# Optimization experiments

Measured on AMD Instinct MI355X. Metric: run time of the kernel, lower is better.

## Reference

```python
import jax, jax.numpy as jnp
import numpy as np
import math

D_MODEL = 2048
N_HEADS = 16
HEAD_DIM = D_MODEL // N_HEADS
ROPE_THETA = 10000.0
EPS = 1e-5


def _rope_cos_sin(seq_len, dim, theta):
    inv_freq = 1.0 / theta ** (jnp.arange(0, dim, 2, dtype=jnp.float32) / dim)  # [dim/2]
    t = jnp.arange(seq_len, dtype=jnp.float32)
    freqs = jnp.outer(t, inv_freq)  # [S, dim/2]
    return jnp.cos(freqs), jnp.sin(freqs)


def _apply_rope(x, cos, sin):
    # x: [B, S, H, D]; pairs (even, odd) rotated by angle freqs[s, d/2]
    xs = x.reshape(x.shape[:-1] + (x.shape[-1] // 2, 2))
    x0, x1 = xs[..., 0], xs[..., 1]
    c = cos[None, :, None, :]
    s = sin[None, :, None, :]
    out = jnp.stack([x0 * c - x1 * s, x0 * s + x1 * c], axis=-1)
    return out.reshape(x.shape)


def _layernorm(x, w, eps):
    # LayerNorm over last dim, no bias
    mu = jnp.mean(x, axis=-1, keepdims=True)
    var = jnp.mean(jnp.square(x - mu), axis=-1, keepdims=True)
    return (x - mu) * jax.lax.rsqrt(var + eps) * w


def setup_inputs() -> dict:
    key = jax.random.key(0)
    ks = jax.random.split(key, 5)
    B, S = 2, 2048
    w_std = math.sqrt(1.0 / D_MODEL)  # ~xavier for square matrices
    return {
        "x": jax.random.normal(ks[0], (B, S, D_MODEL), dtype=jnp.float32),
        "wq": jax.random.normal(ks[1], (D_MODEL, D_MODEL), dtype=jnp.float32) * w_std,
        "wk": jax.random.normal(ks[2], (D_MODEL, D_MODEL), dtype=jnp.float32) * w_std,
        "wv": jax.random.normal(ks[3], (D_MODEL, D_MODEL), dtype=jnp.float32) * w_std,
        "wo": jax.random.normal(ks[4], (D_MODEL, D_MODEL), dtype=jnp.float32) * w_std,
        "q_norm_w": jnp.ones((HEAD_DIM,), dtype=jnp.float32),
        "k_norm_w": jnp.ones((HEAD_DIM,), dtype=jnp.float32),
        "window_size": 1024,
    }


def reference(x, wq, wk, wv, wo, q_norm_w, k_norm_w, window_size):
    B, S, _ = x.shape
    # bias-free projections (torch Linear: x @ W.T)
    q = (x @ wq.T).reshape(B, S, N_HEADS, HEAD_DIM)
    k = (x @ wk.T).reshape(B, S, N_HEADS, HEAD_DIM)
    v = (x @ wv.T).reshape(B, S, N_HEADS, HEAD_DIM)

    cos, sin = _rope_cos_sin(S, HEAD_DIM, ROPE_THETA)
    q = _apply_rope(q, cos, sin)
    k = _apply_rope(k, cos, sin)

    # per-head QK LayerNorm (no bias)
    q = _layernorm(q, q_norm_w, EPS)
    k = _layernorm(k, k_norm_w, EPS)

    scale = 1.0 / math.sqrt(HEAD_DIM)
    scores = jnp.einsum("bqhd,bkhd->bhqk", q, k) * scale  # [B,H,S,S]

    # sliding-window causal mask: attend to j in [i - window, i]
    i = jnp.arange(S)[:, None]
    j = jnp.arange(S)[None, :]
    allowed = (j <= i) & (j >= i - window_size)
    scores = jnp.where(allowed, scores, -jnp.inf)

    attn = jax.nn.softmax(scores, axis=-1)
    out = jnp.einsum("bhqk,bkhd->bqhd", attn, v).reshape(B, S, D_MODEL)
    return out @ wo.T
```

## Files before the change

### kernel.cpp

```cpp
#include <hip/hip_runtime.h>

typedef __bf16 bfv8 __attribute__((ext_vector_type(8)));
typedef float f32x4 __attribute__((ext_vector_type(4)));

#define DMODEL 2048
#define NHEADS 16
#define HEADD 128
#define SEQ 2048
#define BATCH 2
#define MROWS (BATCH * SEQ)

__device__ __forceinline__ unsigned short f2bf(float f) {
    unsigned int x = __float_as_uint(f);
    x += 0x7fffu + ((x >> 16) & 1u);
    return (unsigned short)(x >> 16);
}
__device__ __forceinline__ float bf2f(unsigned short u) {
    return __uint_as_float((unsigned int)u << 16);
}
__device__ __forceinline__ unsigned int pk2(float a, float b) {
    return (unsigned int)f2bf(a) | ((unsigned int)f2bf(b) << 16);
}

__global__ __launch_bounds__(256) void cvt_f2b(const float* __restrict__ s,
                                               unsigned short* __restrict__ d, int n) {
    int i = (blockIdx.x * 256 + threadIdx.x) * 4;
    if (i >= n) return;
    float4 v = *(const float4*)(s + i);
    ushort4 o;
    o.x = f2bf(v.x); o.y = f2bf(v.y); o.z = f2bf(v.z); o.w = f2bf(v.w);
    *(ushort4*)(d + i) = o;
}

template <int CPRL>
__device__ __forceinline__ void stage_t(const unsigned short* __restrict__ gbase,
                                        unsigned short* lds, size_t strideShorts,
                                        int wave, int lane) {
#pragma unroll
    for (int i = 0; i < 4; ++i) {
        int L = wave * 256 + i * 64 + lane;
        int m = L >> CPRL, c = L & ((1 << CPRL) - 1);
        int g = c ^ (m & 7);
        const unsigned short* gp = gbase + (size_t)m * strideShorts + g * 8;
        __builtin_amdgcn_global_load_lds(
            (const __attribute__((address_space(1))) unsigned int*)gp,
            (__attribute__((address_space(3))) unsigned int*)(lds + (size_t)(wave * 256 + i * 64) * 8),
            16, 0, 0);
    }
}

#define GBK 64

__global__ __launch_bounds__(256) void gemm_qkv(const unsigned short* __restrict__ A,
                                                const unsigned short* __restrict__ Bw,
                                                unsigned short* __restrict__ Qb,
                                                unsigned short* __restrict__ Kb,
                                                unsigned short* __restrict__ VT) {
    __shared__ __align__(16) unsigned short As[128 * 64];
    __shared__ __align__(16) unsigned short Bs[128 * 64];
    const int K = DMODEL;
    int tid  = threadIdx.x;
    int bm   = blockIdx.y * 128, bn = blockIdx.x * 128;
    int wave = tid >> 6, lane = tid & 63;
    int wm   = (wave >> 1) * 64, wn = (wave & 1) * 64;
    int lr   = lane & 15, lg = lane >> 4;

    f32x4 acc[4][4];
    f32x4 z = {0.f, 0.f, 0.f, 0.f};
#pragma unroll
    for (int i = 0; i < 4; ++i)
#pragma unroll
        for (int j = 0; j < 4; ++j) acc[i][j] = z;

    const unsigned short* Ab = A  + (size_t)bm * K;
    const unsigned short* Bb = Bw + (size_t)bn * K;

    for (int k0 = 0; k0 < K; k0 += GBK) {
        __syncthreads();
        stage_t<3>(Ab + k0, As, K, wave, lane);
        stage_t<3>(Bb + k0, Bs, K, wave, lane);
        __syncthreads();
#pragma unroll
        for (int kk = 0; kk < GBK; kk += 32) {
            int ck = (kk >> 3) + lg;
            bfv8 af[4], bf[4];
#pragma unroll
            for (int i = 0; i < 4; ++i)
                af[i] = *(const bfv8*)&As[(wm + i * 16 + lr) * 64 + ((ck ^ (lr & 7))) * 8];
#pragma unroll
            for (int j = 0; j < 4; ++j)
                bf[j] = *(const bfv8*)&Bs[(wn + j * 16 + lr) * 64 + ((ck ^ (lr & 7))) * 8];
#pragma unroll
            for (int i = 0; i < 4; ++i)
#pragma unroll
                for (int j = 0; j < 4; ++j)
                    acc[i][j] = __builtin_amdgcn_mfma_f32_16x16x32_bf16(af[i], bf[j], acc[i][j], 0, 0, 0);
        }
    }
    int orow0 = bm + wm + lg * 4;
    int region = bn >> 11;
    int nloc   = bn & 2047;
    if (region < 2) {
        unsigned short* C = region ? Kb : Qb;
#pragma unroll
        for (int i = 0; i < 4; ++i)
#pragma unroll
            for (int j = 0; j < 4; ++j)
#pragma unroll
                for (int r = 0; r < 4; ++r)
                    C[(size_t)(orow0 + i * 16 + r) * DMODEL + nloc + wn + j * 16 + lr] = f2bf(acc[i][j][r]);
    } else {
#pragma unroll
        for (int i = 0; i < 4; ++i) {
            int row = orow0 + i * 16;
            int bb = row >> 11, ss = row & (SEQ - 1);
#pragma unroll
            for (int j = 0; j < 4; ++j) {
                int col = nloc + wn + j * 16 + lr;
                int hh = col >> 7, dd = col & (HEADD - 1);
                ushort4 o4;
                o4.x = f2bf(acc[i][j][0]);
                o4.y = f2bf(acc[i][j][1]);
                o4.z = f2bf(acc[i][j][2]);
                o4.w = f2bf(acc[i][j][3]);
                *(ushort4*)(VT + ((size_t)((bb * NHEADS + hh) * HEADD + dd)) * SEQ + ss) = o4;
            }
        }
    }
}

__global__ __launch_bounds__(256) void gemm_bt(const unsigned short* __restrict__ A,
                                               const unsigned short* __restrict__ Bw,
                                               float* __restrict__ C,
                                               int M, int N, int K) {
    __shared__ __align__(16) unsigned short As[128 * 64];
    __shared__ __align__(16) unsigned short Bs[128 * 64];
    int tid  = threadIdx.x;
    int bm   = blockIdx.y * 128, bn = blockIdx.x * 128;
    int wave = tid >> 6, lane = tid & 63;
    int wm   = (wave >> 1) * 64, wn = (wave & 1) * 64;
    int lr   = lane & 15, lg = lane >> 4;

    f32x4 acc[4][4];
    f32x4 z = {0.f, 0.f, 0.f, 0.f};
#pragma unroll
    for (int i = 0; i < 4; ++i)
#pragma unroll
        for (int j = 0; j < 4; ++j) acc[i][j] = z;

    const unsigned short* Ab = A  + (size_t)bm * K;
    const unsigned short* Bb = Bw + (size_t)bn * K;

    for (int k0 = 0; k0 < K; k0 += GBK) {
        __syncthreads();
        stage_t<3>(Ab + k0, As, K, wave, lane);
        stage_t<3>(Bb + k0, Bs, K, wave, lane);
        __syncthreads();
#pragma unroll
        for (int kk = 0; kk < GBK; kk += 32) {
            int ck = (kk >> 3) + lg;
            bfv8 af[4], bf[4];
#pragma unroll
            for (int i = 0; i < 4; ++i)
                af[i] = *(const bfv8*)&As[(wm + i * 16 + lr) * 64 + ((ck ^ (lr & 7))) * 8];
#pragma unroll
            for (int j = 0; j < 4; ++j)
                bf[j] = *(const bfv8*)&Bs[(wn + j * 16 + lr) * 64 + ((ck ^ (lr & 7))) * 8];
#pragma unroll
            for (int i = 0; i < 4; ++i)
#pragma unroll
                for (int j = 0; j < 4; ++j)
                    acc[i][j] = __builtin_amdgcn_mfma_f32_16x16x32_bf16(af[i], bf[j], acc[i][j], 0, 0, 0);
        }
    }
    int orow0 = bm + wm + lg * 4;
    int ocol0 = bn + wn + lr;
#pragma unroll
    for (int i = 0; i < 4; ++i)
#pragma unroll
        for (int j = 0; j < 4; ++j)
#pragma unroll
            for (int r = 0; r < 4; ++r)
                C[(size_t)(orow0 + i * 16 + r) * N + ocol0 + j * 16] = acc[i][j][r];
}

__global__ __launch_bounds__(256) void rope_ln_ip(unsigned short* __restrict__ qt,
                                                  unsigned short* __restrict__ kt,
                                                  const float* __restrict__ qw,
                                                  const float* __restrict__ kw) {
    int which = blockIdx.y;
    unsigned short* t = which ? kt : qt;
    const float* w = which ? kw : qw;
    float scale = which ? 1.0f : 0.08838834764831845f;
    int gr   = blockIdx.x * 4 + (threadIdx.x >> 6);
    int lane = threadIdx.x & 63;
    int m = gr >> 4;
    int h = gr & 15;
    int s = m & (SEQ - 1);
    unsigned short* p = t + (size_t)m * DMODEL + h * HEADD + lane * 2;
    ushort2 xv = *(const ushort2*)p;
    float x0 = bf2f(xv.x), x1 = bf2f(xv.y);
    float inv = powf(10000.0f, -(float)lane * (1.0f / 64.0f));
    float ang = (float)s * inv;
    float sn, c;
    sincosf(ang, &sn, &c);
    float y0 = x0 * c - x1 * sn;
    float y1 = x0 * sn + x1 * c;
    float sum = y0 + y1;
    float sq  = y0 * y0 + y1 * y1;
#pragma unroll
    for (int o = 32; o >= 1; o >>= 1) {
        sum += __shfl_xor(sum, o);
        sq  += __shfl_xor(sq, o);
    }
    float mu  = sum * (1.0f / 128.0f);
    float var = sq * (1.0f / 128.0f) - mu * mu;
    float rs  = rsqrtf(var + 1e-5f) * scale;
    float2 wv = *(const float2*)(w + lane * 2);
    ushort2 ov;
    ov.x = f2bf((y0 - mu) * rs * wv.x);
    ov.y = f2bf((y1 - mu) * rs * wv.y);
    *(ushort2*)p = ov;
}

#define AQT 64
#define AKT 64

__global__ __launch_bounds__(256) void attn_mfma(const unsigned short* __restrict__ qb,
                                                 const unsigned short* __restrict__ kb,
                                                 const unsigned short* __restrict__ vt,
                                                 unsigned short* __restrict__ ob,
                                                 const int* __restrict__ wptr) {
    __shared__ __align__(16) unsigned short Ks[64 * 128];
    __shared__ __align__(16) unsigned short Vs[128 * 64];
    __shared__ __align__(16) unsigned short Ps[4 * 16 * 64];
    int tid  = threadIdx.x;
    int wq   = tid >> 6, lane = tid & 63;
    int lm   = lane & 15, lg = lane >> 4;
    int lm7  = lm & 7;
    int gid  = blockIdx.x;
    int xcd  = gid & 7, slot = gid >> 3;
    int bh   = xcd * 4 + (slot >> 5);
    int b    = bh >> 4, h = bh & 15;
    int q0   = (31 - (slot & 31)) * AQT;
    int W    = *wptr;
    unsigned short* PsW = &Ps[wq * 1024];

    bfv8 qa[4];
    {
        const unsigned short* qp = qb + (size_t)(b * SEQ + q0 + wq * 16 + lm) * DMODEL + h * HEADD + lg * 8;
#pragma unroll
        for (int kk = 0; kk < 4; ++kk) qa[kk] = *(const bfv8*)(qp + kk * 32);
    }

    f32x4 o[8];
    f32x4 z = {0.f, 0.f, 0.f, 0.f};
#pragma unroll
    for (int n = 0; n < 8; ++n) o[n] = z;
    float mrow = -1e30f, lrow = 0.f;

    const unsigned short* kbase = kb + (size_t)(b * SEQ) * DMODEL + h * HEADD;
    const unsigned short* vbase = vt + (size_t)((b * NHEADS + h) * HEADD) * SEQ;

    int kt_lo = max(0, q0 - W) & ~(AKT - 1);
    int qi = q0 + wq * 16 + lm;

    for (int kt = kt_lo; kt < q0 + AQT; kt += AKT) {
        __syncthreads();
        stage_t<4>(kbase + (size_t)kt * DMODEL, Ks, DMODEL, wq, lane);
        stage_t<3>(vbase + kt, Vs, SEQ, wq, lane);
        __syncthreads();

        f32x4 s[4];
#pragma unroll
        for (int j = 0; j < 4; ++j) s[j] = z;
#pragma unroll
        for (int kk = 0; kk < 4; ++kk) {
#pragma unroll
            for (int j = 0; j < 4; ++j) {
                int ck = (kk * 4 + lg) ^ lm7;
                bfv8 af = *(const bfv8*)&Ks[(j * 16 + lm) * 128 + ck * 8];
                s[j] = __builtin_amdgcn_mfma_f32_16x16x32_bf16(af, qa[kk], s[j], 0, 0, 0);
            }
        }
        if ((kt + 63 >= q0) || (kt < q0 + 63 - W)) {
#pragma unroll
            for (int j = 0; j < 4; ++j) {
                int kj0 = kt + j * 16 + lg * 4;
#pragma unroll
                for (int r = 0; r < 4; ++r) {
                    bool ok = (kj0 + r <= qi) && (kj0 + r >= qi - W);
                    s[j][r] = ok ? s[j][r] : -1e30f;
                }
            }
        }
        float mx = -1e30f;
#pragma unroll
        for (int j = 0; j < 4; ++j)
#pragma unroll
            for (int r = 0; r < 4; ++r) mx = fmaxf(mx, s[j][r]);
        mx = fmaxf(mx, __shfl_xor(mx, 16));
        mx = fmaxf(mx, __shfl_xor(mx, 32));
        float mnew  = fmaxf(mrow, mx);
        float alpha = __expf(mrow - mnew);
        mrow = mnew;
        float ls = 0.f;
#pragma unroll
        for (int j = 0; j < 4; ++j) {
            float p0 = __expf(s[j][0] - mnew);
            float p1 = __expf(s[j][1] - mnew);
            float p2 = __expf(s[j][2] - mnew);
            float p3 = __expf(s[j][3] - mnew);
            ls += (p0 + p1) + (p2 + p3);
            int c0 = (j * 2 + (lg >> 1)) ^ lm7;
            uint2 wv;
            wv.x = pk2(p0, p1);
            wv.y = pk2(p2, p3);
            *(uint2*)&PsW[lm * 64 + c0 * 8 + (lg & 1) * 4] = wv;
        }
        ls += __shfl_xor(ls, 16);
        ls += __shfl_xor(ls, 32);
        lrow = lrow * alpha + ls;
        float al[4];
#pragma unroll
        for (int r = 0; r < 4; ++r) al[r] = __shfl(alpha, lg * 4 + r);
#pragma unroll
        for (int n = 0; n < 8; ++n)
#pragma unroll
            for (int r = 0; r < 4; ++r) o[n][r] *= al[r];
#pragma unroll
        for (int k2 = 0; k2 < 2; ++k2) {
            int cc = (k2 * 4 + lg) ^ lm7;
            bfv8 pa = *(const bfv8*)&PsW[lm * 64 + cc * 8];
#pragma unroll
            for (int n = 0; n < 8; ++n) {
                bfv8 vf = *(const bfv8*)&Vs[(n * 16 + lm) * 64 + cc * 8];
                o[n] = __builtin_amdgcn_mfma_f32_16x16x32_bf16(pa, vf, o[n], 0, 0, 0);
            }
        }
    }
    float linv[4];
#pragma unroll
    for (int r = 0; r < 4; ++r) linv[r] = 1.0f / __shfl(lrow, lg * 4 + r);
    int qrow = q0 + wq * 16 + lg * 4;
    unsigned short* op = ob + (size_t)(b * SEQ + qrow) * DMODEL + h * HEADD + lm;
#pragma unroll
    for (int n = 0; n < 8; ++n)
#pragma unroll
        for (int r = 0; r < 4; ++r)
            op[(size_t)r * DMODEL + n * 16] = f2bf(o[n][r] * linv[r]);
}

extern "C" void kernel_launch(void* const* d_in, const int* in_sizes, int n_in,
                              void* d_out, int out_size, void* d_ws, size_t ws_size,
                              hipStream_t stream) {
    const float* x   = (const float*)d_in[0];
    const float* wq  = (const float*)d_in[1];
    const float* wk  = (const float*)d_in[2];
    const float* wv  = (const float*)d_in[3];
    const float* wo  = (const float*)d_in[4];
    const float* qnw = (const float*)d_in[5];
    const float* knw = (const float*)d_in[6];
    const int*   wsz = (const int*)d_in[7];
    float* out = (float*)d_out;

    char* ws = (char*)d_ws;
    unsigned short* xb  = (unsigned short*)(ws);
    unsigned short* w1  = (unsigned short*)(ws + 16777216);
    unsigned short* w2  = (unsigned short*)(ws + 25165824);
    unsigned short* w3  = (unsigned short*)(ws + 33554432);
    unsigned short* w4  = (unsigned short*)(ws + 41943040);
    unsigned short* qbf = (unsigned short*)(ws + 50331648);
    unsigned short* kbf = (unsigned short*)(ws + 67108864);
    unsigned short* vtb = (unsigned short*)(ws + 83886080);

    cvt_f2b<<<8192, 256, 0, stream>>>(x,  xb, MROWS * DMODEL);
    cvt_f2b<<<4096, 256, 0, stream>>>(wq, w1, DMODEL * DMODEL);
    cvt_f2b<<<4096, 256, 0, stream>>>(wk, w2, DMODEL * DMODEL);
    cvt_f2b<<<4096, 256, 0, stream>>>(wv, w3, DMODEL * DMODEL);
    cvt_f2b<<<4096, 256, 0, stream>>>(wo, w4, DMODEL * DMODEL);

    gemm_qkv<<<dim3(3 * DMODEL / 128, MROWS / 128), 256, 0, stream>>>(xb, w1, qbf, kbf, vtb);

    rope_ln_ip<<<dim3(MROWS * NHEADS / 4, 2), 256, 0, stream>>>(qbf, kbf, qnw, knw);

    attn_mfma<<<(SEQ / AQT) * NHEADS * BATCH, 256, 0, stream>>>(qbf, kbf, vtb, xb, wsz);

    gemm_bt<<<dim3(DMODEL / 128, MROWS / 128), 256, 0, stream>>>(xb, w4, out, MROWS, DMODEL, DMODEL);
}
```

Measured before the change: 439.8 us.

## Fuse RoPE+LayerNorm into QKV GEMM epilogue, merge conversions, enlarge attention tiles

Five fp32-to-bf16 conversion launches are merged into a single kernel writing one contiguous buffer. The separate RoPE+LayerNorm pass is folded into the QKV GEMM epilogue, using lane shuffles and an LDS row reduction across the two column-half waves. The attention kernel moves from 64 to 128 query and key tiles with two 16-row query groups per wave, and V is now read directly from global memory instead of staged in LDS. This removes launches and a full Q/K read-write pass, but raises register pressure and makes V loads uncached global reads.

```diff
diff --git a/kernel.cpp b/kernel.cpp
--- a/kernel.cpp
+++ b/kernel.cpp
@@ -15,47 +15,57 @@
     x += 0x7fffu + ((x >> 16) & 1u);
     return (unsigned short)(x >> 16);
 }
-__device__ __forceinline__ float bf2f(unsigned short u) {
-    return __uint_as_float((unsigned int)u << 16);
-}
 __device__ __forceinline__ unsigned int pk2(float a, float b) {
     return (unsigned int)f2bf(a) | ((unsigned int)f2bf(b) << 16);
 }
 
-__global__ __launch_bounds__(256) void cvt_f2b(const float* __restrict__ s,
-                                               unsigned short* __restrict__ d, int n) {
-    int i = (blockIdx.x * 256 + threadIdx.x) * 4;
-    if (i >= n) return;
+__global__ __launch_bounds__(256) void cvt_all(const float* __restrict__ x,
+                                               const float* __restrict__ wq,
+                                               const float* __restrict__ wk,
+                                               const float* __restrict__ wv,
+                                               const float* __restrict__ wo,
+                                               unsigned short* __restrict__ dst) {
+    int bid = blockIdx.x;
+    const float* s;
+    int off;
+    if (bid < 8192)       { s = x;  off = bid; }
+    else if (bid < 12288) { s = wq; off = bid - 8192; }
+    else if (bid < 16384) { s = wk; off = bid - 12288; }
+    else if (bid < 20480) { s = wv; off = bid - 16384; }
+    else                  { s = wo; off = bid - 20480; }
+    int i = off * 1024 + threadIdx.x * 4;
     float4 v = *(const float4*)(s + i);
     ushort4 o;
     o.x = f2bf(v.x); o.y = f2bf(v.y); o.z = f2bf(v.z); o.w = f2bf(v.w);
-    *(ushort4*)(d + i) = o;
-}
-
-template <int CPRL>
-__device__ __forceinline__ void stage_t(const unsigned short* __restrict__ gbase,
+    *(ushort4*)(dst + (size_t)bid * 1024 + threadIdx.x * 4) = o;
+}
+
+template <int CPRL, int ITERS>
+__device__ __forceinline__ void stage_n(const unsigned short* __restrict__ gbase,
                                         unsigned short* lds, size_t strideShorts,
                                         int wave, int lane) {
 #pragma unroll
-    for (int i = 0; i < 4; ++i) {
-        int L = wave * 256 + i * 64 + lane;
+    for (int i = 0; i < ITERS; ++i) {
+        int L = wave * (64 * ITERS) + i * 64 + lane;
         int m = L >> CPRL, c = L & ((1 << CPRL) - 1);
         int g = c ^ (m & 7);
         const unsigned short* gp = gbase + (size_t)m * strideShorts + g * 8;
         __builtin_amdgcn_global_load_lds(
             (const __attribute__((address_space(1))) unsigned int*)gp,
-            (__attribute__((address_space(3))) unsigned int*)(lds + (size_t)(wave * 256 + i * 64) * 8),
+            (__attribute__((address_space(3))) unsigned int*)(lds + (size_t)(wave * (64 * ITERS) + i * 64) * 8),
             16, 0, 0);
     }
 }
 
 #define GBK 64
 
-__global__ __launch_bounds__(256) void gemm_qkv(const unsigned short* __restrict__ A,
-                                                const unsigned short* __restrict__ Bw,
-                                                unsigned short* __restrict__ Qb,
-                                                unsigned short* __restrict__ Kb,
-                                                unsigned short* __restrict__ VT) {
+__global__ __launch_bounds__(256, 4) void gemm_qkv(const unsigned short* __restrict__ A,
+                                                   const unsigned short* __restrict__ Bw,
+                                                   unsigned short* __restrict__ Qb,
+                                                   unsigned short* __restrict__ Kb,
+                                                   unsigned short* __restrict__ VT,
+                                                   const float* __restrict__ qnw,
+                                                   const float* __restrict__ knw) {
     __shared__ __align__(16) unsigned short As[128 * 64];
     __shared__ __align__(16) unsigned short Bs[128 * 64];
     const int K = DMODEL;
@@ -77,8 +87,8 @@
 
     for (int k0 = 0; k0 < K; k0 += GBK) {
         __syncthreads();
-        stage_t<3>(Ab + k0, As, K, wave, lane);
-        stage_t<3>(Bb + k0, Bs, K, wave, lane);
+        stage_n<3, 4>(Ab + k0, As, K, wave, lane);
+        stage_n<3, 4>(Bb + k0, Bs, K, wave, lane);
         __syncthreads();
 #pragma unroll
         for (int kk = 0; kk < GBK; kk += 32) {
@@ -86,10 +96,10 @@
             bfv8 af[4], bf[4];
 #pragma unroll
             for (int i = 0; i < 4; ++i)
-                af[i] = *(const bfv8*)&As[(wm + i * 16 + lr) * 64 + ((ck ^ (lr & 7))) * 8];
+                af[i] = *(const bfv8*)&As[(wm + i * 16 + lr) * 64 + (ck ^ (lr & 7)) * 8];
 #pragma unroll
             for (int j = 0; j < 4; ++j)
-                bf[j] = *(const bfv8*)&Bs[(wn + j * 16 + lr) * 64 + ((ck ^ (lr & 7))) * 8];
+                bf[j] = *(const bfv8*)&Bs[(wn + j * 16 + lr) * 64 + (ck ^ (lr & 7)) * 8];
 #pragma unroll
             for (int i = 0; i < 4; ++i)
 #pragma unroll
@@ -97,26 +107,82 @@
                     acc[i][j] = __builtin_amdgcn_mfma_f32_16x16x32_bf16(af[i], bf[j], acc[i][j], 0, 0, 0);
         }
     }
-    int orow0 = bm + wm + lg * 4;
+    int lm = lr;
     int region = bn >> 11;
     int nloc   = bn & 2047;
     if (region < 2) {
         unsigned short* C = region ? Kb : Qb;
+        const float* nw = region ? knw : qnw;
+        float scale = region ? 1.0f : 0.08838834764831845f;
+        float invf[4], wnw[4];
+#pragma unroll
+        for (int j = 0; j < 4; ++j) {
+            int dd = wn + j * 16 + lm;
+            invf[j] = exp2f(-(float)(dd >> 1) * 0.20762050593046f);
+            wnw[j] = nw[dd];
+        }
+        int sbase = (bm & (SEQ - 1)) + wm + lg * 4;
 #pragma unroll
         for (int i = 0; i < 4; ++i)
 #pragma unroll
-            for (int j = 0; j < 4; ++j)
-#pragma unroll
-                for (int r = 0; r < 4; ++r)
-                    C[(size_t)(orow0 + i * 16 + r) * DMODEL + nloc + wn + j * 16 + lr] = f2bf(acc[i][j][r]);
+            for (int r = 0; r < 4; ++r) {
+                float sv = (float)(sbase + i * 16 + r);
+#pragma unroll
+                for (int j = 0; j < 4; ++j) {
+                    float sn, cs;
+                    __sincosf(sv * invf[j], &sn, &cs);
+                    float x0 = acc[i][j][r];
+                    float x1 = __shfl_xor(x0, 1);
+                    acc[i][j][r] = (lm & 1) ? fmaf(x1, sn, x0 * cs)
+                                            : fmaf(x0, cs, -(x1 * sn));
+                }
+            }
+        float* red = (float*)As;
+        int half = wn >> 6;
+        __syncthreads();
+#pragma unroll
+        for (int i = 0; i < 4; ++i)
+#pragma unroll
+            for (int r = 0; r < 4; ++r) {
+                float a0 = acc[i][0][r], a1 = acc[i][1][r], a2 = acc[i][2][r], a3 = acc[i][3][r];
+                float s1 = (a0 + a1) + (a2 + a3);
+                float s2 = fmaf(a0, a0, fmaf(a1, a1, fmaf(a2, a2, a3 * a3)));
+#pragma unroll
+                for (int msk = 1; msk <= 8; msk <<= 1) {
+                    s1 += __shfl_xor(s1, msk);
+                    s2 += __shfl_xor(s2, msk);
+                }
+                if (lm == 0) {
+                    int rloc = wm + lg * 4 + i * 16 + r;
+                    red[(rloc * 2 + half) * 2 + 0] = s1;
+                    red[(rloc * 2 + half) * 2 + 1] = s2;
+                }
+            }
+        __syncthreads();
+#pragma unroll
+        for (int i = 0; i < 4; ++i)
+#pragma unroll
+            for (int r = 0; r < 4; ++r) {
+                int rloc = wm + lg * 4 + i * 16 + r;
+                float t1 = red[(rloc * 2 + 0) * 2 + 0] + red[(rloc * 2 + 1) * 2 + 0];
+                float t2 = red[(rloc * 2 + 0) * 2 + 1] + red[(rloc * 2 + 1) * 2 + 1];
+                float mu  = t1 * (1.0f / 128.0f);
+                float var = t2 * (1.0f / 128.0f) - mu * mu;
+                float rs  = rsqrtf(var + 1e-5f) * scale;
+                size_t rowoff = (size_t)(bm + rloc) * DMODEL + nloc;
+#pragma unroll
+                for (int j = 0; j < 4; ++j)
+                    C[rowoff + wn + j * 16 + lm] = f2bf((acc[i][j][r] - mu) * rs * wnw[j]);
+            }
     } else {
+        int orow0 = bm + wm + lg * 4;
 #pragma unroll
         for (int i = 0; i < 4; ++i) {
             int row = orow0 + i * 16;
             int bb = row >> 11, ss = row & (SEQ - 1);
 #pragma unroll
             for (int j = 0; j < 4; ++j) {
-                int col = nloc + wn + j * 16 + lr;
+                int col = nloc + wn + j * 16 + lm;
                 int hh = col >> 7, dd = col & (HEADD - 1);
                 ushort4 o4;
                 o4.x = f2bf(acc[i][j][0]);
@@ -153,8 +219,8 @@
 
     for (int k0 = 0; k0 < K; k0 += GBK) {
         __syncthreads();
-        stage_t<3>(Ab + k0, As, K, wave, lane);
-        stage_t<3>(Bb + k0, Bs, K, wave, lane);
+        stage_n<3, 4>(Ab + k0, As, K, wave, lane);
+        stage_n<3, 4>(Bb + k0, Bs, K, wave, lane);
         __syncthreads();
 #pragma unroll
         for (int kk = 0; kk < GBK; kk += 32) {
@@ -162,10 +228,10 @@
             bfv8 af[4], bf[4];
 #pragma unroll
             for (int i = 0; i < 4; ++i)
-                af[i] = *(const bfv8*)&As[(wm + i * 16 + lr) * 64 + ((ck ^ (lr & 7))) * 8];
+                af[i] = *(const bfv8*)&As[(wm + i * 16 + lr) * 64 + (ck ^ (lr & 7)) * 8];
 #pragma unroll
             for (int j = 0; j < 4; ++j)
-                bf[j] = *(const bfv8*)&Bs[(wn + j * 16 + lr) * 64 + ((ck ^ (lr & 7))) * 8];
+                bf[j] = *(const bfv8*)&Bs[(wn + j * 16 + lr) * 64 + (ck ^ (lr & 7)) * 8];
 #pragma unroll
             for (int i = 0; i < 4; ++i)
 #pragma unroll
@@ -184,171 +250,149 @@
                 C[(size_t)(orow0 + i * 16 + r) * N + ocol0 + j * 16] = acc[i][j][r];
 }
 
-__global__ __launch_bounds__(256) void rope_ln_ip(unsigned short* __restrict__ qt,
-                                                  unsigned short* __restrict__ kt,
-                                                  const float* __restrict__ qw,
-                                                  const float* __restrict__ kw) {
-    int which = blockIdx.y;
-    unsigned short* t = which ? kt : qt;
-    const float* w = which ? kw : qw;
-    float scale = which ? 1.0f : 0.08838834764831845f;
-    int gr   = blockIdx.x * 4 + (threadIdx.x >> 6);
-    int lane = threadIdx.x & 63;
-    int m = gr >> 4;
-    int h = gr & 15;
-    int s = m & (SEQ - 1);
-    unsigned short* p = t + (size_t)m * DMODEL + h * HEADD + lane * 2;
-    ushort2 xv = *(const ushort2*)p;
-    float x0 = bf2f(xv.x), x1 = bf2f(xv.y);
-    float inv = powf(10000.0f, -(float)lane * (1.0f / 64.0f));
-    float ang = (float)s * inv;
-    float sn, c;
-    sincosf(ang, &sn, &c);
-    float y0 = x0 * c - x1 * sn;
-    float y1 = x0 * sn + x1 * c;
-    float sum = y0 + y1;
-    float sq  = y0 * y0 + y1 * y1;
-#pragma unroll
-    for (int o = 32; o >= 1; o >>= 1) {
-        sum += __shfl_xor(sum, o);
-        sq  += __shfl_xor(sq, o);
-    }
-    float mu  = sum * (1.0f / 128.0f);
-    float var = sq * (1.0f / 128.0f) - mu * mu;
-    float rs  = rsqrtf(var + 1e-5f) * scale;
-    float2 wv = *(const float2*)(w + lane * 2);
-    ushort2 ov;
-    ov.x = f2bf((y0 - mu) * rs * wv.x);
-    ov.y = f2bf((y1 - mu) * rs * wv.y);
-    *(ushort2*)p = ov;
-}
-
-#define AQT 64
-#define AKT 64
-
-__global__ __launch_bounds__(256) void attn_mfma(const unsigned short* __restrict__ qb,
-                                                 const unsigned short* __restrict__ kb,
-                                                 const unsigned short* __restrict__ vt,
-                                                 unsigned short* __restrict__ ob,
-                                                 const int* __restrict__ wptr) {
-    __shared__ __align__(16) unsigned short Ks[64 * 128];
-    __shared__ __align__(16) unsigned short Vs[128 * 64];
-    __shared__ __align__(16) unsigned short Ps[4 * 16 * 64];
+#define AQT 128
+#define AKT 128
+
+__global__ __launch_bounds__(256, 2) void attn_mfma(const unsigned short* __restrict__ qb,
+                                                    const unsigned short* __restrict__ kb,
+                                                    const unsigned short* __restrict__ vt,
+                                                    unsigned short* __restrict__ ob,
+                                                    const int* __restrict__ wptr) {
+    __shared__ __align__(16) unsigned short Ks[128 * 128];
+    __shared__ __align__(16) unsigned short Ps[4 * 32 * 128];
     int tid  = threadIdx.x;
     int wq   = tid >> 6, lane = tid & 63;
     int lm   = lane & 15, lg = lane >> 4;
     int lm7  = lm & 7;
     int gid  = blockIdx.x;
     int xcd  = gid & 7, slot = gid >> 3;
-    int bh   = xcd * 4 + (slot >> 5);
+    int bh   = xcd * 4 + (slot >> 4);
     int b    = bh >> 4, h = bh & 15;
-    int q0   = (31 - (slot & 31)) * AQT;
+    int q0   = (15 - (slot & 15)) * AQT;
     int W    = *wptr;
-    unsigned short* PsW = &Ps[wq * 1024];
-
-    bfv8 qa[4];
-    {
-        const unsigned short* qp = qb + (size_t)(b * SEQ + q0 + wq * 16 + lm) * DMODEL + h * HEADD + lg * 8;
-#pragma unroll
-        for (int kk = 0; kk < 4; ++kk) qa[kk] = *(const bfv8*)(qp + kk * 32);
-    }
-
-    f32x4 o[8];
+    unsigned short* PsW = &Ps[wq * 32 * 128];
+
+    bfv8 qa[2][4];
+#pragma unroll
+    for (int nq = 0; nq < 2; ++nq) {
+        const unsigned short* qp = qb + (size_t)(b * SEQ + q0 + wq * 32 + nq * 16 + lm) * DMODEL + h * HEADD + lg * 8;
+#pragma unroll
+        for (int kk = 0; kk < 4; ++kk) qa[nq][kk] = *(const bfv8*)(qp + kk * 32);
+    }
+
+    f32x4 o[2][8];
     f32x4 z = {0.f, 0.f, 0.f, 0.f};
 #pragma unroll
-    for (int n = 0; n < 8; ++n) o[n] = z;
-    float mrow = -1e30f, lrow = 0.f;
+    for (int mq = 0; mq < 2; ++mq)
+#pragma unroll
+        for (int n = 0; n < 8; ++n) o[mq][n] = z;
+    float mrow[2] = {-1e30f, -1e30f}, lrow[2] = {0.f, 0.f};
 
     const unsigned short* kbase = kb + (size_t)(b * SEQ) * DMODEL + h * HEADD;
     const unsigned short* vbase = vt + (size_t)((b * NHEADS + h) * HEADD) * SEQ;
 
     int kt_lo = max(0, q0 - W) & ~(AKT - 1);
-    int qi = q0 + wq * 16 + lm;
+    int qi0 = q0 + wq * 32 + lm;
 
     for (int kt = kt_lo; kt < q0 + AQT; kt += AKT) {
         __syncthreads();
-        stage_t<4>(kbase + (size_t)kt * DMODEL, Ks, DMODEL, wq, lane);
-        stage_t<3>(vbase + kt, Vs, SEQ, wq, lane);
-        __syncthreads();
-
-        f32x4 s[4];
-#pragma unroll
-        for (int j = 0; j < 4; ++j) s[j] = z;
-#pragma unroll
-        for (int kk = 0; kk < 4; ++kk) {
-#pragma unroll
-            for (int j = 0; j < 4; ++j) {
-                int ck = (kk * 4 + lg) ^ lm7;
-                bfv8 af = *(const bfv8*)&Ks[(j * 16 + lm) * 128 + ck * 8];
-                s[j] = __builtin_amdgcn_mfma_f32_16x16x32_bf16(af, qa[kk], s[j], 0, 0, 0);
-            }
-        }
-        if ((kt + 63 >= q0) || (kt < q0 + 63 - W)) {
-#pragma unroll
-            for (int j = 0; j < 4; ++j) {
+        stage_n<4, 8>(kbase + (size_t)kt * DMODEL, Ks, DMODEL, wq, lane);
+        __syncthreads();
+
+        f32x4 s[8][2];
+#pragma unroll
+        for (int j = 0; j < 8; ++j) { s[j][0] = z; s[j][1] = z; }
+#pragma unroll
+        for (int kk = 0; kk < 4; ++kk)
+#pragma unroll
+            for (int j = 0; j < 8; ++j) {
+                bfv8 af = *(const bfv8*)&Ks[(j * 16 + lm) * 128 + (((kk * 4 + lg)) ^ lm7) * 8];
+                s[j][0] = __builtin_amdgcn_mfma_f32_16x16x32_bf16(af, qa[0][kk], s[j][0], 0, 0, 0);
+                s[j][1] = __builtin_amdgcn_mfma_f32_16x16x32_bf16(af, qa[1][kk], s[j][1], 0, 0, 0);
+            }
+        if ((kt + AKT - 1 > q0) || (kt < q0 + AQT - 1 - W)) {
+#pragma unroll
+            for (int j = 0; j < 8; ++j) {
                 int kj0 = kt + j * 16 + lg * 4;
 #pragma unroll
-                for (int r = 0; r < 4; ++r) {
-                    bool ok = (kj0 + r <= qi) && (kj0 + r >= qi - W);
-                    s[j][r] = ok ? s[j][r] : -1e30f;
+                for (int nq = 0; nq < 2; ++nq) {
+                    int qi = qi0 + nq * 16;
+#pragma unroll
+                    for (int r = 0; r < 4; ++r) {
+                        bool ok = (kj0 + r <= qi) && (kj0 + r >= qi - W);
+                        s[j][nq][r] = ok ? s[j][nq][r] : -1e30f;
+                    }
                 }
             }
         }
-        float mx = -1e30f;
-#pragma unroll
-        for (int j = 0; j < 4; ++j)
-#pragma unroll
-            for (int r = 0; r < 4; ++r) mx = fmaxf(mx, s[j][r]);
-        mx = fmaxf(mx, __shfl_xor(mx, 16));
-        mx = fmaxf(mx, __shfl_xor(mx, 32));
-        float mnew  = fmaxf(mrow, mx);
-        float alpha = __expf(mrow - mnew);
-        mrow = mnew;
-        float ls = 0.f;
-#pragma unroll
-        for (int j = 0; j < 4; ++j) {
-            float p0 = __expf(s[j][0] - mnew);
-            float p1 = __expf(s[j][1] - mnew);
-            float p2 = __expf(s[j][2] - mnew);
-            float p3 = __expf(s[j][3] - mnew);
-            ls += (p0 + p1) + (p2 + p3);
-            int c0 = (j * 2 + (lg >> 1)) ^ lm7;
-            uint2 wv;
-            wv.x = pk2(p0, p1);
-            wv.y = pk2(p2, p3);
-            *(uint2*)&PsW[lm * 64 + c0 * 8 + (lg & 1) * 4] = wv;
-        }
-        ls += __shfl_xor(ls, 16);
-        ls += __shfl_xor(ls, 32);
-        lrow = lrow * alpha + ls;
-        float al[4];
-#pragma unroll
-        for (int r = 0; r < 4; ++r) al[r] = __shfl(alpha, lg * 4 + r);
+        float alpha[2];
+#pragma unroll
+        for (int nq = 0; nq < 2; ++nq) {
+            float mx = -1e30f;
+#pragma unroll
+            for (int j = 0; j < 8; ++j)
+#pragma unroll
+                for (int r = 0; r < 4; ++r) mx = fmaxf(mx, s[j][nq][r]);
+            mx = fmaxf(mx, __shfl_xor(mx, 16));
+            mx = fmaxf(mx, __shfl_xor(mx, 32));
+            float mnew = fmaxf(mrow[nq], mx);
+            alpha[nq] = __expf(mrow[nq] - mnew);
+            mrow[nq] = mnew;
+            float ls = 0.f;
+#pragma unroll
+            for (int j = 0; j < 8; ++j) {
+                float p0 = __expf(s[j][nq][0] - mnew);
+                float p1 = __expf(s[j][nq][1] - mnew);
+                float p2 = __expf(s[j][nq][2] - mnew);
+                float p3 = __expf(s[j][nq][3] - mnew);
+                ls += (p0 + p1) + (p2 + p3);
+                int c0 = (j * 2 + (lg >> 1)) ^ lm7;
+                uint2 wv;
+                wv.x = pk2(p0, p1);
+                wv.y = pk2(p2, p3);
+                *(uint2*)&PsW[(nq * 16 + lm) * 128 + c0 * 8 + (lg & 1) * 4] = wv;
+            }
+            ls += __shfl_xor(ls, 16);
+            ls += __shfl_xor(ls, 32);
+            lrow[nq] = lrow[nq] * alpha[nq] + ls;
+        }
+#pragma unroll
+        for (int mq = 0; mq < 2; ++mq)
+#pragma unroll
+            for (int r = 0; r < 4; ++r) {
+                float al = __shfl(alpha[mq], lg * 4 + r);
+#pragma unroll
+                for (int n = 0; n < 8; ++n) o[mq][n][r] *= al;
+            }
+#pragma unroll
+        for (int k2 = 0; k2 < 4; ++k2) {
+            int cc = (k2 * 4 + lg) ^ lm7;
+            bfv8 pa0 = *(const bfv8*)&PsW[lm * 128 + cc * 8];
+            bfv8 pa1 = *(const bfv8*)&PsW[(16 + lm) * 128 + cc * 8];
+            bfv8 vf[8];
+#pragma unroll
+            for (int n = 0; n < 8; ++n)
+                vf[n] = *(const bfv8*)(vbase + (size_t)(n * 16 + lm) * SEQ + kt + (k2 * 4 + lg) * 8);
+#pragma unroll
+            for (int n = 0; n < 8; ++n) {
+                o[0][n] = __builtin_amdgcn_mfma_f32_16x16x32_bf16(pa0, vf[n], o[0][n], 0, 0, 0);
+                o[1][n] = __builtin_amdgcn_mfma_f32_16x16x32_bf16(pa1, vf[n], o[1][n], 0, 0, 0);
+            }
+        }
+    }
+#pragma unroll
+    for (int mq = 0; mq < 2; ++mq) {
+        float linv[4];
+#pragma unroll
+        for (int r = 0; r < 4; ++r) linv[r] = 1.0f / __shfl(lrow[mq], lg * 4 + r);
+        int qrow = q0 + wq * 32 + mq * 16 + lg * 4;
+        unsigned short* op = ob + (size_t)(b * SEQ + qrow) * DMODEL + h * HEADD + lm;
 #pragma unroll
         for (int n = 0; n < 8; ++n)
 #pragma unroll
-            for (int r = 0; r < 4; ++r) o[n][r] *= al[r];
-#pragma unroll
-        for (int k2 = 0; k2 < 2; ++k2) {
-            int cc = (k2 * 4 + lg) ^ lm7;
-            bfv8 pa = *(const bfv8*)&PsW[lm * 64 + cc * 8];
-#pragma unroll
-            for (int n = 0; n < 8; ++n) {
-                bfv8 vf = *(const bfv8*)&Vs[(n * 16 + lm) * 64 + cc * 8];
-                o[n] = __builtin_amdgcn_mfma_f32_16x16x32_bf16(pa, vf, o[n], 0, 0, 0);
-            }
-        }
-    }
-    float linv[4];
-#pragma unroll
-    for (int r = 0; r < 4; ++r) linv[r] = 1.0f / __shfl(lrow, lg * 4 + r);
-    int qrow = q0 + wq * 16 + lg * 4;
-    unsigned short* op = ob + (size_t)(b * SEQ + qrow) * DMODEL + h * HEADD + lm;
-#pragma unroll
-    for (int n = 0; n < 8; ++n)
-#pragma unroll
-        for (int r = 0; r < 4; ++r)
-            op[(size_t)r * DMODEL + n * 16] = f2bf(o[n][r] * linv[r]);
+            for (int r = 0; r < 4; ++r)
+                op[(size_t)r * DMODEL + n * 16] = f2bf(o[mq][n][r] * linv[r]);
+    }
 }
 
 extern "C" void kernel_launch(void* const* d_in, const int* in_sizes, int n_in,
@@ -367,22 +411,14 @@
     char* ws = (char*)d_ws;
     unsigned short* xb  = (unsigned short*)(ws);
     unsigned short* w1  = (unsigned short*)(ws + 16777216);
-    unsigned short* w2  = (unsigned short*)(ws + 25165824);
-    unsigned short* w3  = (unsigned short*)(ws + 33554432);
     unsigned short* w4  = (unsigned short*)(ws + 41943040);
     unsigned short* qbf = (unsigned short*)(ws + 50331648);
     unsigned short* kbf = (unsigned short*)(ws + 67108864);
     unsigned short* vtb = (unsigned short*)(ws + 83886080);
 
-    cvt_f2b<<<8192, 256, 0, stream>>>(x,  xb, MROWS * DMODEL);
-    cvt_f2b<<<4096, 256, 0, stream>>>(wq, w1, DMODEL * DMODEL);
-    cvt_f2b<<<4096, 256, 0, stream>>>(wk, w2, DMODEL * DMODEL);
-    cvt_f2b<<<4096, 256, 0, stream>>>(wv, w3, DMODEL * DMODEL);
-    cvt_f2b<<<4096, 256, 0, stream>>>(wo, w4, DMODEL * DMODEL);
-
-    gemm_qkv<<<dim3(3 * DMODEL / 128, MROWS / 128), 256, 0, stream>>>(xb, w1, qbf, kbf, vtb);
-
-    rope_ln_ip<<<dim3(MROWS * NHEADS / 4, 2), 256, 0, stream>>>(qbf, kbf, qnw, knw);
+    cvt_all<<<24576, 256, 0, stream>>>(x, wq, wk, wv, wo, xb);
+
+    gemm_qkv<<<dim3(3 * DMODEL / 128, MROWS / 128), 256, 0, stream>>>(xb, w1, qbf, kbf, vtb, qnw, knw);
 
     attn_mfma<<<(SEQ / AQT) * NHEADS * BATCH, 256, 0, stream>>>(qbf, kbf, vtb, xb, wsz);
 
```

Result: no change. 444.8 us (+1.1%).
